# Kernel tuning notes

Measured on AMD Instinct MI355X. Metric: run time of the kernel, lower is better.

Reference implementation:

```python
import jax, jax.numpy as jnp
import numpy as np

N_NODES = 100000
N_EDGES = 1600000
NODE_D = 64
EDGE_D = 48
U_D = 32
N_GRAPHS = 64
HIDDEN = 128
OUT_D = 64
IN_D = NODE_D + EDGE_D + U_D  # 144


def setup_inputs() -> dict:
    key = jax.random.key(0)
    ks = jax.random.split(key, 10)
    x = jax.random.normal(ks[0], (N_NODES, NODE_D), dtype=jnp.float32)
    edge_index = jax.random.randint(ks[1], (2, N_EDGES), 0, N_NODES, dtype=jnp.int64)
    edge_attr = jax.random.normal(ks[2], (N_EDGES, EDGE_D), dtype=jnp.float32)
    u = jax.random.normal(ks[3], (N_GRAPHS, U_D), dtype=jnp.float32)
    batch = jnp.sort(jax.random.randint(ks[4], (N_NODES,), 0, N_GRAPHS, dtype=jnp.int64))
    # FCNN params: Linear(144,128) -> relu -> Linear(128,128) -> relu -> Linear(128,64)
    W1 = jax.random.normal(ks[5], (IN_D, HIDDEN), dtype=jnp.float32) / np.sqrt(IN_D)
    b1 = jnp.zeros((HIDDEN,), dtype=jnp.float32)
    W2 = jax.random.normal(ks[6], (HIDDEN, HIDDEN), dtype=jnp.float32) / np.sqrt(HIDDEN)
    b2 = jnp.zeros((HIDDEN,), dtype=jnp.float32)
    W3 = jax.random.normal(ks[7], (HIDDEN, OUT_D), dtype=jnp.float32) / np.sqrt(HIDDEN)
    b3 = jnp.zeros((OUT_D,), dtype=jnp.float32)
    return {"x": x, "edge_index": edge_index, "edge_attr": edge_attr, "u": u,
            "batch": batch, "W1": W1, "b1": b1, "W2": W2, "b2": b2, "W3": W3, "b3": b3}


def reference(x, edge_index, edge_attr, u, batch, W1, b1, W2, b2, W3, b3):
    n = x.shape[0]
    seg = edge_index[0]  # source node per edge
    # scatter_mean(edge_attr, edge_index[0], dim=0) -> [N, edge_d]
    sums = jax.ops.segment_sum(edge_attr, seg, num_segments=n)
    cnt = jax.ops.segment_sum(jnp.ones((edge_attr.shape[0],), edge_attr.dtype), seg, num_segments=n)
    v_e = sums / jnp.maximum(cnt, 1.0)[:, None]  # mean, 0 for empty segments
    comb = jnp.concatenate([x, v_e, u[batch]], axis=1)  # [N, 144]
    h = jax.nn.relu(comb @ W1 + b1)
    h = jax.nn.relu(h @ W2 + b2)
    return h @ W3 + b3
```

## Files before the change

kernel.cpp:

```cpp
#include <hip/hip_runtime.h>
#include <hip/hip_bf16.h>

#define NN 100000
#define NE 1600000
#define NODE_D 64
#define EDGE_D 48
#define E16 64
#define U_D 32
#define IN_D 144
#define HID 128
#define OUT_D 64
#define BM 64
#define S0 152
#define SCAN_BS 1024
#define SCAN_NB ((NN + SCAN_BS - 1) / SCAN_BS)
#define W1K 160
#define NW1 (HID * W1K)
#define NW2 (HID * HID)
#define NW3 (OUT_D * HID)
#define NWTOT (NW1 + NW2 + NW3)
#define CH 16

typedef __attribute__((ext_vector_type(8))) short bf16x8;
typedef __attribute__((ext_vector_type(4))) float f32x4;
typedef __attribute__((ext_vector_type(4))) unsigned int u32x4;

__device__ __forceinline__ short f2bs(float f) {
  union { __hip_bfloat16 h; short s; } v;
  v.h = __float2bfloat16(f);
  return v.s;
}
__device__ __forceinline__ float blo(unsigned int pk) {
  union { unsigned int u; float f; } v; v.u = pk << 16; return v.f;
}
__device__ __forceinline__ float bhi(unsigned int pk) {
  union { unsigned int u; float f; } v; v.u = pk & 0xffff0000u; return v.f;
}
__device__ __forceinline__ unsigned pk2(float a, float b) {
  return (unsigned)(unsigned short)f2bs(a) | ((unsigned)(unsigned short)f2bs(b) << 16);
}

__device__ __forceinline__ void st4(unsigned short* p, float4 v) {
  *reinterpret_cast<uint2*>(p) = make_uint2(pk2(v.x, v.y), pk2(v.z, v.w));
}

__global__ __launch_bounds__(256) void setup_kernel(
    int* __restrict__ hist,
    const float* __restrict__ W1, const float* __restrict__ W2,
    const float* __restrict__ W3, unsigned short* __restrict__ Wp) {
  const int b = blockIdx.x, tid = threadIdx.x;
  if (b < SCAN_NB) {
    int base = b * SCAN_BS + tid * 4;
    if (base + 3 < NN) {
      *reinterpret_cast<int4*>(&hist[base]) = make_int4(0, 0, 0, 0);
    } else {
      for (int k = 0; k < 4; ++k)
        if (base + k < NN) hist[base + k] = 0;
    }
    return;
  }
  int gid = (b - SCAN_NB) * 256 + tid;
  if (gid >= NWTOT) return;
  float v;
  if (gid < NW1) {
    int n = gid / W1K, k = gid - n * W1K;
    v = (k < IN_D) ? W1[(size_t)k * HID + n] : 0.f;
  } else if (gid < NW1 + NW2) {
    int i2 = gid - NW1;
    int n = i2 >> 7, k = i2 & 127;
    v = W2[(size_t)k * HID + n];
  } else {
    int i3 = gid - NW1 - NW2;
    int n = i3 >> 7, k = i3 & 127;
    v = W3[(size_t)k * OUT_D + n];
  }
  Wp[gid] = (unsigned short)f2bs(v);
}

__global__ __launch_bounds__(256) void hist_kernel(const int* __restrict__ src,
                                                   int* __restrict__ hist) {
  int i = blockIdx.x * 256 + threadIdx.x;
  if (i * 4 >= NE) return;
  int4 s = reinterpret_cast<const int4*>(src)[i];
  atomicAdd(&hist[s.x], 1);
  atomicAdd(&hist[s.y], 1);
  atomicAdd(&hist[s.z], 1);
  atomicAdd(&hist[s.w], 1);
}

__global__ __launch_bounds__(256) void bsum_kernel(const int* __restrict__ hist,
                                                   int* __restrict__ bsum) {
  const int b = blockIdx.x, tid = threadIdx.x;
  const int base = b * SCAN_BS + tid * 4;
  int4 v = make_int4(0, 0, 0, 0);
  if (base + 3 < NN) v = *reinterpret_cast<const int4*>(&hist[base]);
  else {
    int t[4] = {0, 0, 0, 0};
    for (int k = 0; k < 4; ++k) if (base + k < NN) t[k] = hist[base + k];
    v = make_int4(t[0], t[1], t[2], t[3]);
  }
  int s = v.x + v.y + v.z + v.w;
  for (int d = 32; d; d >>= 1) s += __shfl_down(s, d, 64);
  __shared__ int ws[4];
  if ((tid & 63) == 0) ws[tid >> 6] = s;
  __syncthreads();
  if (tid == 0) bsum[b] = ws[0] + ws[1] + ws[2] + ws[3];
}

__global__ __launch_bounds__(128) void bscan_kernel(const int* __restrict__ bsum,
                                                    int* __restrict__ bpre) {
  const int t = threadIdx.x;
  const int lane = t & 63, wave = t >> 6;
  int v = (t < SCAN_NB) ? bsum[t] : 0;
  int incl = v;
  for (int d = 1; d < 64; d <<= 1) {
    int q = __shfl_up(incl, d, 64);
    if (lane >= d) incl += q;
  }
  __shared__ int wtot[2];
  if (lane == 63) wtot[wave] = incl;
  __syncthreads();
  int add = (wave == 1) ? wtot[0] : 0;
  if (t < SCAN_NB) bpre[t] = incl - v + add;
}

__global__ __launch_bounds__(256) void offsets_kernel(const int* __restrict__ hist,
                                                      const int* __restrict__ bpre,
                                                      int* __restrict__ offsets,
                                                      int* __restrict__ cursor) {
  const int b = blockIdx.x, tid = threadIdx.x;
  const int base = b * SCAN_BS + tid * 4;
  const int lane = tid & 63, wave = tid >> 6;
  int4 v = make_int4(0, 0, 0, 0);
  if (base + 3 < NN) v = *reinterpret_cast<const int4*>(&hist[base]);
  else {
    int t[4] = {0, 0, 0, 0};
    for (int k = 0; k < 4; ++k) if (base + k < NN) t[k] = hist[base + k];
    v = make_int4(t[0], t[1], t[2], t[3]);
  }
  const int tsum = v.x + v.y + v.z + v.w;
  int incl = tsum;
  for (int d = 1; d < 64; d <<= 1) {
    int q = __shfl_up(incl, d, 64);
    if (lane >= d) incl += q;
  }
  __shared__ int ws[4];
  __shared__ int wpre[4];
  if (lane == 63) ws[wave] = incl;
  __syncthreads();
  if (tid == 0) {
    int r = 0;
    for (int w = 0; w < 4; ++w) { wpre[w] = r; r += ws[w]; }
  }
  __syncthreads();
  int run = bpre[b] + wpre[wave] + incl - tsum;
  int vals[4] = {v.x, v.y, v.z, v.w};
  for (int k = 0; k < 4; ++k) {
    int i = base + k;
    if (i < NN) { offsets[i] = run; cursor[i] = run; run += vals[k]; }
  }
}

__global__ __launch_bounds__(256) void pack_scatter_kernel(
    const int* __restrict__ src, const float* __restrict__ ea,
    int* __restrict__ cursor, unsigned short* __restrict__ ea16) {
  __shared__ float stage[4][CH * EDGE_D];
  __shared__ int posbuf[4][CH];
  const int wid = threadIdx.x >> 6;
  const int lane = threadIdx.x & 63;
  float* st = stage[wid];
  int* pos = posbuf[wid];
  const int nchunks = NE / CH;
  const int stride = gridDim.x * 4;
  for (int ch = blockIdx.x * 4 + wid; ch < nchunks; ch += stride) {
    const int e0 = ch * CH;
    if (lane < CH) {
      int s = src[e0 + lane];
      pos[lane] = atomicAdd(&cursor[s], 1);
    }
    const float4* gsrc = reinterpret_cast<const float4*>(ea + (size_t)e0 * EDGE_D);
    float4 v0 = gsrc[lane];
    float4 v1 = gsrc[lane + 64];
    float4 v2 = gsrc[lane + 128];
    float4* stv = reinterpret_cast<float4*>(st);
    stv[lane] = v0;
    stv[lane + 64] = v1;
    stv[lane + 128] = v2;
#pragma unroll
    for (int pass = 0; pass < 2; ++pass) {
      int t = pass * 64 + lane;
      int r = t >> 3, c = t & 7;
      u32x4 w = {0u, 0u, 0u, 0u};
      if (c < 6) {
        const float* f = st + r * EDGE_D + c * 8;
        w.x = pk2(f[0], f[1]);
        w.y = pk2(f[2], f[3]);
        w.z = pk2(f[4], f[5]);
        w.w = pk2(f[6], f[7]);
      }
      int p = pos[r];
      *reinterpret_cast<u32x4*>(ea16 + (size_t)p * E16 + c * 8) = w;
    }
  }
}

__global__ __launch_bounds__(256) void fused_kernel(
    const float* __restrict__ x, const unsigned short* __restrict__ ea16,
    const float* __restrict__ u, const int* __restrict__ batch,
    const int* __restrict__ hist, const int* __restrict__ offsets,
    const unsigned short* __restrict__ Wp,
    const float* __restrict__ b1, const float* __restrict__ b2,
    const float* __restrict__ b3, float* __restrict__ out) {
  __shared__ __align__(16) unsigned short act[BM][S0];

  const int tid = threadIdx.x;
  const int lane = tid & 63;
  const int wid = tid >> 6;
  const int lr = lane & 15;
  const int lg = lane >> 4;
  const int node0 = blockIdx.x * BM;

  const unsigned short* Wp1 = Wp;
  const unsigned short* Wp2 = Wp + NW1;
  const unsigned short* Wp3 = Wp + NW1 + NW2;

  const bf16x8 az = {0, 0, 0, 0, 0, 0, 0, 0};

  for (int i = tid; i < BM * (NODE_D / 4); i += 256) {
    int r = i >> 4, q = i & 15;
    int node = node0 + r;
    float4 v = make_float4(0.f, 0.f, 0.f, 0.f);
    if (node < NN) v = reinterpret_cast<const float4*>(x)[(size_t)node * 16 + q];
    st4(&act[r][q * 4], v);
  }
  for (int i = tid; i < BM * (U_D / 4); i += 256) {
    int r = i >> 3, q = i & 7;
    int node = node0 + r;
    float4 v = make_float4(0.f, 0.f, 0.f, 0.f);
    if (node < NN) {
      int b = batch[node];
      v = reinterpret_cast<const float4*>(u)[(size_t)b * 8 + q];
    }
    st4(&act[r][NODE_D + EDGE_D + q * 4], v);
  }

  {
    const int g = tid >> 4;
    const int c = tid & 15;
    for (int i = 0; i < 4; ++i) {
      const int nl = g * 4 + i;
      const int node = node0 + nl;
      int deg = 0, off = 0;
      if (node < NN) { deg = hist[node]; off = offsets[node]; }
      const unsigned short* rp = ea16 + (size_t)off * E16 + c * 4;
      float4 a0 = make_float4(0.f, 0.f, 0.f, 0.f);
      float4 a1 = make_float4(0.f, 0.f, 0.f, 0.f);
      int j = 0;
      for (; j + 7 < deg; j += 8) {
        uint2 w0 = *reinterpret_cast<const uint2*>(rp + (size_t)(j + 0) * E16);
        uint2 w1 = *reinterpret_cast<const uint2*>(rp + (size_t)(j + 1) * E16);
        uint2 w2 = *reinterpret_cast<const uint2*>(rp + (size_t)(j + 2) * E16);
        uint2 w3 = *reinterpret_cast<const uint2*>(rp + (size_t)(j + 3) * E16);
        uint2 w4 = *reinterpret_cast<const uint2*>(rp + (size_t)(j + 4) * E16);
        uint2 w5 = *reinterpret_cast<const uint2*>(rp + (size_t)(j + 5) * E16);
        uint2 w6 = *reinterpret_cast<const uint2*>(rp + (size_t)(j + 6) * E16);
        uint2 w7 = *reinterpret_cast<const uint2*>(rp + (size_t)(j + 7) * E16);
        a0.x += blo(w0.x) + blo(w1.x) + blo(w2.x) + blo(w3.x);
        a0.y += bhi(w0.x) + bhi(w1.x) + bhi(w2.x) + bhi(w3.x);
        a0.z += blo(w0.y) + blo(w1.y) + blo(w2.y) + blo(w3.y);
        a0.w += bhi(w0.y) + bhi(w1.y) + bhi(w2.y) + bhi(w3.y);
        a1.x += blo(w4.x) + blo(w5.x) + blo(w6.x) + blo(w7.x);
        a1.y += bhi(w4.x) + bhi(w5.x) + bhi(w6.x) + bhi(w7.x);
        a1.z += blo(w4.y) + blo(w5.y) + blo(w6.y) + blo(w7.y);
        a1.w += bhi(w4.y) + bhi(w5.y) + bhi(w6.y) + bhi(w7.y);
      }
      for (; j < deg; ++j) {
        uint2 w0 = *reinterpret_cast<const uint2*>(rp + (size_t)j * E16);
        a0.x += blo(w0.x); a0.y += bhi(w0.x);
        a0.z += blo(w0.y); a0.w += bhi(w0.y);
      }
      float inv = (deg > 0) ? 1.0f / (float)deg : 0.0f;
      if (c < 12 && node < NN)
        st4(&act[nl][NODE_D + c * 4],
            make_float4((a0.x + a1.x) * inv, (a0.y + a1.y) * inv,
                        (a0.z + a1.z) * inv, (a0.w + a1.w) * inv));
    }
  }
  __syncthreads();

  {
    const int n0 = wid * 32;
    bf16x8 wf[5][2];
#pragma unroll
    for (int t = 0; t < 5; ++t)
#pragma unroll
      for (int nf = 0; nf < 2; ++nf)
        wf[t][nf] = *reinterpret_cast<const bf16x8*>(
            &Wp1[(size_t)(n0 + nf * 16 + lr) * W1K + t * 32 + lg * 8]);
    float bias0 = b1[n0 + lr], bias1 = b1[n0 + 16 + lr];
    f32x4 acc[4][2];
#pragma unroll
    for (int mf = 0; mf < 4; ++mf) {
      acc[mf][0] = (f32x4){bias0, bias0, bias0, bias0};
      acc[mf][1] = (f32x4){bias1, bias1, bias1, bias1};
    }
#pragma unroll
    for (int t = 0; t < 5; ++t) {
#pragma unroll
      for (int mf = 0; mf < 4; ++mf) {
        bf16x8 a;
        if (t < 4) {
          a = *reinterpret_cast<const bf16x8*>(&act[mf * 16 + lr][t * 32 + lg * 8]);
        } else {
          a = az;
          if (lg < 2)
            a = *reinterpret_cast<const bf16x8*>(&act[mf * 16 + lr][128 + lg * 8]);
        }
        acc[mf][0] = __builtin_amdgcn_mfma_f32_16x16x32_bf16(a, wf[t][0], acc[mf][0], 0, 0, 0);
        acc[mf][1] = __builtin_amdgcn_mfma_f32_16x16x32_bf16(a, wf[t][1], acc[mf][1], 0, 0, 0);
      }
    }
    __syncthreads();
#pragma unroll
    for (int mf = 0; mf < 4; ++mf)
#pragma unroll
      for (int nf = 0; nf < 2; ++nf)
#pragma unroll
        for (int r = 0; r < 4; ++r)
          act[mf * 16 + lg * 4 + r][n0 + nf * 16 + lr] =
              (unsigned short)f2bs(fmaxf(acc[mf][nf][r], 0.f));
  }
  __syncthreads();

  {
    const int n0 = wid * 32;
    bf16x8 wf[4][2];
#pragma unroll
    for (int t = 0; t < 4; ++t)
#pragma unroll
      for (int nf = 0; nf < 2; ++nf)
        wf[t][nf] = *reinterpret_cast<const bf16x8*>(
            &Wp2[(size_t)(n0 + nf * 16 + lr) * HID + t * 32 + lg * 8]);
    float bias0 = b2[n0 + lr], bias1 = b2[n0 + 16 + lr];
    f32x4 acc[4][2];
#pragma unroll
    for (int mf = 0; mf < 4; ++mf) {
      acc[mf][0] = (f32x4){bias0, bias0, bias0, bias0};
      acc[mf][1] = (f32x4){bias1, bias1, bias1, bias1};
    }
#pragma unroll
    for (int t = 0; t < 4; ++t) {
#pragma unroll
      for (int mf = 0; mf < 4; ++mf) {
        bf16x8 a = *reinterpret_cast<const bf16x8*>(&act[mf * 16 + lr][t * 32 + lg * 8]);
        acc[mf][0] = __builtin_amdgcn_mfma_f32_16x16x32_bf16(a, wf[t][0], acc[mf][0], 0, 0, 0);
        acc[mf][1] = __builtin_amdgcn_mfma_f32_16x16x32_bf16(a, wf[t][1], acc[mf][1], 0, 0, 0);
      }
    }
    __syncthreads();
#pragma unroll
    for (int mf = 0; mf < 4; ++mf)
#pragma unroll
      for (int nf = 0; nf < 2; ++nf)
#pragma unroll
        for (int r = 0; r < 4; ++r)
          act[mf * 16 + lg * 4 + r][n0 + nf * 16 + lr] =
              (unsigned short)f2bs(fmaxf(acc[mf][nf][r], 0.f));
  }
  __syncthreads();

  {
    const int n0 = wid * 16;
    bf16x8 wf[4];
#pragma unroll
    for (int t = 0; t < 4; ++t)
      wf[t] = *reinterpret_cast<const bf16x8*>(
          &Wp3[(size_t)(n0 + lr) * HID + t * 32 + lg * 8]);
    float bias = b3[n0 + lr];
    f32x4 acc[4];
#pragma unroll
    for (int mf = 0; mf < 4; ++mf) acc[mf] = (f32x4){bias, bias, bias, bias};
#pragma unroll
    for (int t = 0; t < 4; ++t) {
#pragma unroll
      for (int mf = 0; mf < 4; ++mf) {
        bf16x8 a = *reinterpret_cast<const bf16x8*>(&act[mf * 16 + lr][t * 32 + lg * 8]);
        acc[mf] = __builtin_amdgcn_mfma_f32_16x16x32_bf16(a, wf[t], acc[mf], 0, 0, 0);
      }
    }
#pragma unroll
    for (int mf = 0; mf < 4; ++mf)
#pragma unroll
      for (int r = 0; r < 4; ++r) {
        int node = node0 + mf * 16 + lg * 4 + r;
        if (node < NN) out[(size_t)node * OUT_D + n0 + lr] = acc[mf][r];
      }
  }
}

extern "C" void kernel_launch(void* const* d_in, const int* in_sizes, int n_in,
                              void* d_out, int out_size, void* d_ws, size_t ws_size,
                              hipStream_t stream) {
  const float* x   = (const float*)d_in[0];
  const int* ei    = (const int*)d_in[1];
  const float* ea  = (const float*)d_in[2];
  const float* u   = (const float*)d_in[3];
  const int* batch = (const int*)d_in[4];
  const float* W1  = (const float*)d_in[5];
  const float* b1  = (const float*)d_in[6];
  const float* W2  = (const float*)d_in[7];
  const float* b2  = (const float*)d_in[8];
  const float* W3  = (const float*)d_in[9];
  const float* b3  = (const float*)d_in[10];
  float* out = (float*)d_out;

  unsigned short* ea16 = (unsigned short*)d_ws;
  int* hist    = (int*)(ea16 + (size_t)NE * E16);
  int* offsets = hist + NN;
  int* cursor  = offsets + NN;
  int* bsum    = cursor + NN;
  int* bpre    = bsum + SCAN_NB;
  unsigned short* Wp = (unsigned short*)(bpre + SCAN_NB + 60);

  const int wblocks = (NWTOT + 255) / 256;
  const int e4blocks = (NE / 4 + 255) / 256;
  setup_kernel<<<SCAN_NB + wblocks, 256, 0, stream>>>(hist, W1, W2, W3, Wp);
  hist_kernel<<<e4blocks, 256, 0, stream>>>(ei, hist);
  bsum_kernel<<<SCAN_NB, 256, 0, stream>>>(hist, bsum);
  bscan_kernel<<<1, 128, 0, stream>>>(bsum, bpre);
  offsets_kernel<<<SCAN_NB, 256, 0, stream>>>(hist, bpre, offsets, cursor);
  pack_scatter_kernel<<<2048, 256, 0, stream>>>(ei, ea, cursor, ea16);
  fused_kernel<<<(NN + BM - 1) / BM, 256, 0, stream>>>(
      x, ea16, u, batch, hist, offsets, Wp, b1, b2, b3, out);
}
```

Before: 281.8 us.

## Fold block-prefix scan into offsets kernel and widen pack-scatter chunks

```diff
diff --git a/kernel.cpp b/kernel.cpp
--- a/kernel.cpp
+++ b/kernel.cpp
@@ -19,7 +19,7 @@
 #define NW2 (HID * HID)
 #define NW3 (OUT_D * HID)
 #define NWTOT (NW1 + NW2 + NW3)
-#define CH 16
+#define CH 32
 
 typedef __attribute__((ext_vector_type(8))) short bf16x8;
 typedef __attribute__((ext_vector_type(4))) float f32x4;
@@ -107,30 +107,22 @@
   if (tid == 0) bsum[b] = ws[0] + ws[1] + ws[2] + ws[3];
 }
 
-__global__ __launch_bounds__(128) void bscan_kernel(const int* __restrict__ bsum,
-                                                    int* __restrict__ bpre) {
-  const int t = threadIdx.x;
-  const int lane = t & 63, wave = t >> 6;
-  int v = (t < SCAN_NB) ? bsum[t] : 0;
-  int incl = v;
-  for (int d = 1; d < 64; d <<= 1) {
-    int q = __shfl_up(incl, d, 64);
-    if (lane >= d) incl += q;
-  }
-  __shared__ int wtot[2];
-  if (lane == 63) wtot[wave] = incl;
-  __syncthreads();
-  int add = (wave == 1) ? wtot[0] : 0;
-  if (t < SCAN_NB) bpre[t] = incl - v + add;
-}
-
 __global__ __launch_bounds__(256) void offsets_kernel(const int* __restrict__ hist,
-                                                      const int* __restrict__ bpre,
+                                                      const int* __restrict__ bsum,
                                                       int* __restrict__ offsets,
                                                       int* __restrict__ cursor) {
   const int b = blockIdx.x, tid = threadIdx.x;
   const int base = b * SCAN_BS + tid * 4;
   const int lane = tid & 63, wave = tid >> 6;
+  __shared__ int bprefix;
+  __shared__ int ws[4];
+  __shared__ int wpre[4];
+  if (wave == 0) {
+    int s = 0;
+    for (int i = lane; i < b; i += 64) s += bsum[i];
+    for (int d = 32; d; d >>= 1) s += __shfl_down(s, d, 64);
+    if (lane == 0) bprefix = s;
+  }
   int4 v = make_int4(0, 0, 0, 0);
   if (base + 3 < NN) v = *reinterpret_cast<const int4*>(&hist[base]);
   else {
@@ -144,8 +136,6 @@
     int q = __shfl_up(incl, d, 64);
     if (lane >= d) incl += q;
   }
-  __shared__ int ws[4];
-  __shared__ int wpre[4];
   if (lane == 63) ws[wave] = incl;
   __syncthreads();
   if (tid == 0) {
@@ -153,7 +143,7 @@
     for (int w = 0; w < 4; ++w) { wpre[w] = r; r += ws[w]; }
   }
   __syncthreads();
-  int run = bpre[b] + wpre[wave] + incl - tsum;
+  int run = bprefix + wpre[wave] + incl - tsum;
   int vals[4] = {v.x, v.y, v.z, v.w};
   for (int k = 0; k < 4; ++k) {
     int i = base + k;
@@ -179,15 +169,16 @@
       pos[lane] = atomicAdd(&cursor[s], 1);
     }
     const float4* gsrc = reinterpret_cast<const float4*>(ea + (size_t)e0 * EDGE_D);
-    float4 v0 = gsrc[lane];
-    float4 v1 = gsrc[lane + 64];
-    float4 v2 = gsrc[lane + 128];
+    float4 v[6];
+#pragma unroll
+    for (int k = 0; k < 6; ++k) v[k] = gsrc[lane + k * 64];
     float4* stv = reinterpret_cast<float4*>(st);
-    stv[lane] = v0;
-    stv[lane + 64] = v1;
-    stv[lane + 128] = v2;
-#pragma unroll
-    for (int pass = 0; pass < 2; ++pass) {
+#pragma unroll
+    for (int k = 0; k < 6; ++k) stv[lane + k * 64] = v[k];
+    asm volatile("s_waitcnt lgkmcnt(0)" ::: "memory");
+    __builtin_amdgcn_sched_barrier(0);
+#pragma unroll
+    for (int pass = 0; pass < 4; ++pass) {
       int t = pass * 64 + lane;
       int r = t >> 3, c = t & 7;
       u32x4 w = {0u, 0u, 0u, 0u};
@@ -201,6 +192,8 @@
       int p = pos[r];
       *reinterpret_cast<u32x4*>(ea16 + (size_t)p * E16 + c * 8) = w;
     }
+    asm volatile("s_waitcnt lgkmcnt(0)" ::: "memory");
+    __builtin_amdgcn_sched_barrier(0);
   }
 }
 
@@ -419,17 +412,15 @@
   int* offsets = hist + NN;
   int* cursor  = offsets + NN;
   int* bsum    = cursor + NN;
-  int* bpre    = bsum + SCAN_NB;
-  unsigned short* Wp = (unsigned short*)(bpre + SCAN_NB + 60);
+  unsigned short* Wp = (unsigned short*)(bsum + SCAN_NB + 62);
 
   const int wblocks = (NWTOT + 255) / 256;
   const int e4blocks = (NE / 4 + 255) / 256;
   setup_kernel<<<SCAN_NB + wblocks, 256, 0, stream>>>(hist, W1, W2, W3, Wp);
   hist_kernel<<<e4blocks, 256, 0, stream>>>(ei, hist);
   bsum_kernel<<<SCAN_NB, 256, 0, stream>>>(hist, bsum);
-  bscan_kernel<<<1, 128, 0, stream>>>(bsum, bpre);
-  offsets_kernel<<<SCAN_NB, 256, 0, stream>>>(hist, bpre, offsets, cursor);
-  pack_scatter_kernel<<<2048, 256, 0, stream>>>(ei, ea, cursor, ea16);
+  offsets_kernel<<<SCAN_NB, 256, 0, stream>>>(hist, bsum, offsets, cursor);
+  pack_scatter_kernel<<<1536, 256, 0, stream>>>(ei, ea, cursor, ea16);
   fused_kernel<<<(NN + BM - 1) / BM, 256, 0, stream>>>(
       x, ea16, u, batch, hist, offsets, Wp, b1, b2, b3, out);
 }
```

Result: no change. 277.7 us (-1.5%).
